# Optimization experiments

Hardware: AMD Instinct MI355X
Metric: run time of the kernel (lower is better)

The kernel has to match this reference:

```python
import jax, jax.numpy as jnp
import numpy as np

H, C = 8, 640            # n_heads, sentence_size (per-head out channels)
HC = H * C               # 5120 concatenated head width
NS, NW, NSEC = 8192, 65536, 1024   # sentences, words, sections
EW, ES, ESEC = 131072, 262144, 16384
WORD, SENT, SECT = 300, 640, 512
FFN_HID = 2048


def setup_inputs() -> dict:
    key = jax.random.key(0)
    ks = jax.random.split(key, 32)
    f = lambda k, sh: (jax.random.normal(k, sh, jnp.float32) * 0.02)
    ri = jax.random.randint
    inp = {}
    inp['Hs'] = jax.random.normal(ks[0], (NS, SENT), jnp.float32)
    inp['Hw'] = jax.random.normal(ks[1], (NW, WORD), jnp.float32)
    inp['HS'] = jax.random.normal(ks[2], (NSEC, SECT), jnp.float32)
    # edge_index convention: row 0 = source nodes, row 1 = target (sentence) nodes
    inp['w2s'] = jnp.stack([ri(ks[3], (EW,), 0, NW), ri(ks[4], (EW,), 0, NS)]).astype(jnp.int32)
    inp['s2s'] = jnp.stack([ri(ks[5], (ES,), 0, NS), ri(ks[6], (ES,), 0, NS)]).astype(jnp.int32)
    inp['S2s'] = jnp.stack([ri(ks[7], (ESEC,), 0, NSEC), ri(ks[8], (ESEC,), 0, NS)]).astype(jnp.int32)
    # gat_w: bipartite (word -> sentence)
    inp['Ww_src'] = f(ks[9], (WORD, HC)); inp['Ww_dst'] = f(ks[10], (SENT, HC))
    inp['aw_src'] = f(ks[11], (H, C)); inp['aw_dst'] = f(ks[12], (H, C)); inp['bw'] = f(ks[13], (HC,))
    # gat_s: sentence -> sentence (shared lin for src/dst)
    inp['Ws'] = f(ks[14], (SENT, HC))
    inp['as_src'] = f(ks[15], (H, C)); inp['as_dst'] = f(ks[16], (H, C)); inp['bs'] = f(ks[17], (HC,))
    # gat_S: bipartite (section -> sentence)
    inp['WS_src'] = f(ks[18], (SECT, HC)); inp['WS_dst'] = f(ks[19], (SENT, HC))
    inp['aS_src'] = f(ks[20], (H, C)); inp['aS_dst'] = f(ks[21], (H, C)); inp['bS'] = f(ks[22], (HC,))
    # fusion gates
    inp['F1_w'] = f(ks[23], (2 * HC, HC)); inp['F1_b'] = f(ks[24], (HC,))
    inp['F2_w'] = f(ks[25], (2 * HC, HC)); inp['F2_b'] = f(ks[26], (HC,))
    # FFN
    inp['l1_w'] = f(ks[27], (HC, FFN_HID)); inp['l1_b'] = f(ks[28], (FFN_HID,))
    inp['l2_w'] = f(ks[29], (FFN_HID, SENT)); inp['l2_b'] = f(ks[30], (SENT,))
    return inp


def _gat(xs, xd, Wsrc, Wdst, asrc, adst, b, edge_index):
    """PyG-style GATConv (concat heads), bipartite (xs -> xd)."""
    N = xd.shape[0]
    hs = (xs @ Wsrc).reshape(-1, H, C)          # [Nsrc,H,C]
    hd = (xd @ Wdst).reshape(-1, H, C)          # [Ndst,H,C]
    al_s = jnp.einsum('nhc,hc->nh', hs, asrc)   # [Nsrc,H]
    al_d = jnp.einsum('nhc,hc->nh', hd, adst)   # [Ndst,H]
    src, dst = edge_index[0], edge_index[1]
    e = jax.nn.leaky_relu(al_s[src] + al_d[dst], negative_slope=0.2)  # [E,H]
    m = jax.ops.segment_max(e, dst, num_segments=N)                   # segment-stable softmax
    ex = jnp.exp(e - m[dst])
    den = jax.ops.segment_sum(ex, dst, num_segments=N)
    alpha = ex / (den[dst] + 1e-16)
    out = jax.ops.segment_sum(hs[src] * alpha[:, :, None], dst, num_segments=N)
    return out.reshape(N, HC) + b


def _fusion(X, Y, W, b):
    Z = jax.nn.sigmoid(jnp.concatenate([X, Y], axis=-1) @ W + b)
    return Z * X + (1.0 - Z) * Y


def reference(Hs, Hw, HS, w2s, s2s, S2s,
              Ww_src, Ww_dst, aw_src, aw_dst, bw,
              Ws, as_src, as_dst, bs,
              WS_src, WS_dst, aS_src, aS_dst, bS,
              F1_w, F1_b, F2_w, F2_b,
              l1_w, l1_b, l2_w, l2_b):
    Uw = jax.nn.elu(_gat(Hw, Hs, Ww_src, Ww_dst, aw_src, aw_dst, bw, w2s))
    Us = jax.nn.elu(_gat(Hs, Hs, Ws, Ws, as_src, as_dst, bs, s2s))
    US = jax.nn.elu(_gat(HS, Hs, WS_src, WS_dst, aS_src, aS_dst, bS, S2s))
    U1 = _fusion(Uw, Us, F1_w, F1_b)
    U2 = _fusion(U1, US, F2_w, F2_b)
    return (U2 @ l1_w + l1_b) @ l2_w + l2_b + Hs
```

## Files before the change

kernel.cpp:

```cpp
#include <hip/hip_runtime.h>
#include <cstdint>
#include <cstddef>

typedef __attribute__((ext_vector_type(8))) __bf16 bf16x8;
typedef __attribute__((ext_vector_type(4))) float f32x4;

static constexpr int kNS   = 8192;
static constexpr int kNW   = 65536;
static constexpr int kNSEC = 1024;
static constexpr int kEW   = 131072;
static constexpr int kES   = 262144;
static constexpr int kESEC = 16384;

__device__ __forceinline__ float eluf(float x)  { return x > 0.f ? x : (__expf(x) - 1.f); }
__device__ __forceinline__ float sigmf(float x) { return 1.f / (1.f + __expf(-x)); }

__device__ __forceinline__ void gload16(const __bf16* g, __bf16* l) {
  __builtin_amdgcn_global_load_lds((const __attribute__((address_space(1))) unsigned int*)g,
                                   (__attribute__((address_space(3))) unsigned int*)l,
                                   16, 0, 0);
}

__global__ __launch_bounds__(256) void conv_transpose(const float* __restrict__ W, int K, int N,
                                                      __bf16* __restrict__ Wt, int KP) {
  __shared__ float t[64][33];
  const int nb = blockIdx.x * 32, kb = blockIdx.y * 64;
  const int tx = threadIdx.x & 31, ty = threadIdx.x >> 5;
#pragma unroll
  for (int i = ty; i < 64; i += 8) {
    const int k = kb + i;
    t[i][tx] = (k < K) ? W[(long)k * N + nb + tx] : 0.f;
  }
  __syncthreads();
  union BU { __bf16 b; unsigned short u; };
#pragma unroll
  for (int i = ty; i < 32; i += 8) {
    BU b0, b1;
    b0.b = (__bf16)t[tx * 2][i];
    b1.b = (__bf16)t[tx * 2 + 1][i];
    const unsigned int pk = ((unsigned int)b1.u << 16) | b0.u;
    *(unsigned int*)(Wt + (long)(nb + i) * KP + kb + tx * 2) = pk;
  }
}

__global__ __launch_bounds__(256) void conv_bf(const float* __restrict__ in, __bf16* __restrict__ outb, long n) {
  long i = (long)blockIdx.x * blockDim.x + threadIdx.x;
  if (i < n) outb[i] = (__bf16)in[i];
}

__global__ __launch_bounds__(256) void head_vecs(const float* __restrict__ W, const float* __restrict__ a,
                                                 float* __restrict__ outv, int Kd, int KP) {
  const int h = blockIdx.x;
  const int lane = threadIdx.x & 63;
  const int k = blockIdx.y * 4 + (threadIdx.x >> 6);
  float s = 0.f;
  if (k < Kd) {
    const float* wr = W + (long)k * 5120 + h * 640;
    const float* ar = a + h * 640;
    for (int c = lane; c < 640; c += 64) s += wr[c] * ar[c];
  }
  for (int o2 = 32; o2; o2 >>= 1) s += __shfl_down(s, o2);
  if (lane == 0) outv[h * KP + k] = (k < Kd) ? s : 0.f;
}

__global__ __launch_bounds__(256) void comb_bias(const float* __restrict__ l1_b, const float* __restrict__ l2_w,
                                                 const float* __restrict__ l2_b, float* __restrict__ bc) {
  const int n = blockIdx.x * 256 + threadIdx.x;
  if (n >= 640) return;
  float s = l2_b[n];
  for (int k = 0; k < 2048; ++k) s += l1_b[k] * l2_w[(long)k * 640 + n];
  bc[n] = s;
}

__global__ __launch_bounds__(256) void att_logits(const float* __restrict__ X, int ldx, int Kd,
                                                  const float* __restrict__ vec, int KP,
                                                  float* __restrict__ outl, int N) {
  const int lane = threadIdx.x & 63;
  const int node = blockIdx.x * 4 + (threadIdx.x >> 6);
  if (node >= N) return;
  const float* xr = X + (long)node * ldx;
  float p[8];
#pragma unroll
  for (int h = 0; h < 8; ++h) p[h] = 0.f;
  for (int k = lane; k < Kd; k += 64) {
    const float xv = xr[k];
#pragma unroll
    for (int h = 0; h < 8; ++h) p[h] += xv * vec[h * KP + k];
  }
#pragma unroll
  for (int h = 0; h < 8; ++h) {
    float v = p[h];
    for (int o2 = 32; o2; o2 >>= 1) v += __shfl_down(v, o2);
    if (lane == 0) outl[(long)node * 8 + h] = v;
  }
}

__global__ __launch_bounds__(256) void att_logits4(const float* __restrict__ X,
                                                   const float* __restrict__ v0, const float* __restrict__ v1,
                                                   const float* __restrict__ v2, const float* __restrict__ v3,
                                                   float* __restrict__ o0, float* __restrict__ o1,
                                                   float* __restrict__ o2, float* __restrict__ o3, int N) {
  const int lane = threadIdx.x & 63;
  const int node = blockIdx.x * 4 + (threadIdx.x >> 6);
  if (node >= N) return;
  const float* xr = X + (long)node * 640;
  float p[4][8];
#pragma unroll
  for (int s = 0; s < 4; ++s)
#pragma unroll
    for (int h = 0; h < 8; ++h) p[s][h] = 0.f;
  for (int k = lane; k < 640; k += 64) {
    const float xv = xr[k];
#pragma unroll
    for (int h = 0; h < 8; ++h) {
      p[0][h] += xv * v0[h * 640 + k];
      p[1][h] += xv * v1[h * 640 + k];
      p[2][h] += xv * v2[h * 640 + k];
      p[3][h] += xv * v3[h * 640 + k];
    }
  }
  float* outs[4] = {o0, o1, o2, o3};
#pragma unroll
  for (int s = 0; s < 4; ++s)
#pragma unroll
    for (int h = 0; h < 8; ++h) {
      float v = p[s][h];
      for (int o2v = 32; o2v; o2v >>= 1) v += __shfl_down(v, o2v);
      if (lane == 0) outs[s][(long)node * 8 + h] = v;
    }
}

__global__ __launch_bounds__(256) void edge_count(const int* __restrict__ dst, int E, int* __restrict__ cnt) {
  const int gid = blockIdx.x * blockDim.x + threadIdx.x;
  if (gid < E) atomicAdd(&cnt[dst[gid]], 1);
}

__global__ __launch_bounds__(1024) void scan_off(const int* __restrict__ cnt, int* __restrict__ offo) {
  __shared__ int part[1024];
  const int tid = threadIdx.x;
  const int base = tid * 8;
  int loc[8];
  int s = 0;
#pragma unroll
  for (int i = 0; i < 8; ++i) { loc[i] = s; s += cnt[base + i]; }
  part[tid] = s;
  __syncthreads();
  for (int d2 = 1; d2 < 1024; d2 <<= 1) {
    int v = (tid >= d2) ? part[tid - d2] : 0;
    __syncthreads();
    part[tid] += v;
    __syncthreads();
  }
  const int pre = (tid > 0) ? part[tid - 1] : 0;
#pragma unroll
  for (int i = 0; i < 8; ++i) offo[base + i] = pre + loc[i];
  if (tid == 1023) offo[8192] = part[1023];
}

__global__ __launch_bounds__(256) void edge_fill(const int* __restrict__ src, const int* __restrict__ dst, int E,
                                                 const int* __restrict__ offo, int* __restrict__ cur,
                                                 int* __restrict__ ssrc) {
  const int gid = blockIdx.x * blockDim.x + threadIdx.x;
  if (gid < E) {
    const int d = dst[gid];
    const int p = offo[d] + atomicAdd(&cur[d], 1);
    ssrc[p] = src[gid];
  }
}

template <int FPAD, int F, bool XPH, bool BIASELU>
__global__ __launch_bounds__(256) void gat_agg(const int* __restrict__ seg_off, const int* __restrict__ ssrc,
                                               const float* __restrict__ als, const float* __restrict__ ald,
                                               const float* __restrict__ X, int ldx,
                                               __bf16* __restrict__ outp, int ldo,
                                               const float* __restrict__ bias) {
  constexpr int C4 = F / 4;
  constexpr int ITEMS = 8 * C4;
  constexpr int L = (ITEMS + 255) / 256;
  const int d = blockIdx.x;
  const int tid = threadIdx.x;
  const int o0 = seg_off[d], o1 = seg_off[d + 1];
  const int deg = o1 - o0;
  __shared__ float exl[64][8];
  __shared__ int ssl[64];
  __shared__ float aldd[8];
  __shared__ float den_s[8];
  if (tid < 8) { aldd[tid] = ald[(long)d * 8 + tid]; den_s[tid] = 0.f; }
  f32x4 acc[L];
  int hh[L], xo[L], oo[L];
  bool vld[L];
#pragma unroll
  for (int l = 0; l < L; ++l) {
    const int idx = tid + l * 256;
    vld[l] = (idx < ITEMS);
    const int h = vld[l] ? (idx / C4) : 0;
    const int c = vld[l] ? (idx - h * C4) : 0;
    hh[l] = h;
    xo[l] = (XPH ? h * F : 0) + c * 4;
    oo[l] = h * FPAD + c * 4;
#pragma unroll
    for (int r = 0; r < 4; ++r) acc[l][r] = 0.f;
  }
  __syncthreads();
  for (int base = 0; base < deg; base += 64) {
    const int nc = min(64, deg - base);
    if (tid < nc) ssl[tid] = ssrc[o0 + base + tid];
    __syncthreads();
    for (int t = tid; t < nc * 8; t += 256) {
      const int e = t >> 3, h = t & 7;
      float v = als[(long)ssl[e] * 8 + h] + aldd[h];
      v = v > 0.f ? v : 0.2f * v;
      exl[e][h] = __expf(v);
    }
    __syncthreads();
    if (tid < 8) {
      float s = 0.f;
      for (int e = 0; e < nc; ++e) s += exl[e][tid];
      den_s[tid] += s;
    }
    for (int e = 0; e < nc; ++e) {
      const float* xr = X + (long)ssl[e] * ldx;
      const float* ex8 = exl[e];
#pragma unroll
      for (int l = 0; l < L; ++l)
        if (vld[l]) {
          const f32x4 v = *(const f32x4*)(xr + xo[l]);
          acc[l] += ex8[hh[l]] * v;
        }
    }
    __syncthreads();
  }
#pragma unroll
  for (int l = 0; l < L; ++l) {
    if (!vld[l]) continue;
    const float dinv = 1.f / (den_s[hh[l]] + 1e-16f);
#pragma unroll
    for (int j = 0; j < 4; ++j) {
      float r = acc[l][j] * dinv;
      if constexpr (BIASELU) { r += bias[oo[l] + j]; r = eluf(r); }
      outp[(long)d * ldo + oo[l] + j] = (__bf16)r;
    }
  }
}

template <int EPI>
__global__ __launch_bounds__(256) void gemm_bt(
    const __bf16* __restrict__ A, int lda, const __bf16* __restrict__ A2, int ksplit,
    const __bf16* __restrict__ Bt, int ldb, int K,
    void* __restrict__ Cout, int ldc,
    const float* __restrict__ bias,
    const __bf16* __restrict__ Xg, const __bf16* __restrict__ Yg, int ldxy,
    const float* __restrict__ Res, int ldres,
    long a_zs, long bt_zs, long c_zs, int b_zs) {
  __shared__ __bf16 sA[2][128 * 32];
  __shared__ __bf16 sB[2][128 * 32];
  const int tid = threadIdx.x;
  const int z = blockIdx.z;
  const int m0 = blockIdx.y * 128, n0 = blockIdx.x * 128;
  const __bf16* Ab = A + (long)z * a_zs;
  const __bf16* A2b = A2 ? A2 + (long)z * a_zs : nullptr;
  const __bf16* Btb = Bt + (long)z * bt_zs;
  const int lane = tid & 63;
  const int wv = tid >> 6, wr = wv >> 1, wc = wv & 1;
  const int fr = lane & 15, fq = lane >> 4;

  const int r0 = tid >> 2, r1 = r0 + 64;
  const int csw = (((tid & 3) ^ ((r0 >> 1) & 3)) * 8);
  const int ldst0 = tid * 8;
  const int ldst1 = 2048 + tid * 8;

  f32x4 acc[4][4];
#pragma unroll
  for (int i = 0; i < 4; ++i)
#pragma unroll
    for (int j = 0; j < 4; ++j)
#pragma unroll
      for (int r = 0; r < 4; ++r) acc[i][j][r] = 0.f;

  const int fsw = (fq ^ ((fr >> 1) & 3)) * 8;
  int aof[4], bof[4];
#pragma unroll
  for (int i = 0; i < 4; ++i) {
    aof[i] = (wr * 64 + i * 16 + fr) * 32 + fsw;
    bof[i] = (wc * 64 + i * 16 + fr) * 32 + fsw;
  }

  const int nkt = K >> 5;
  auto stage = [&](int buf, int kt) {
    const int k0 = kt * 32;
    const __bf16* As = Ab;
    int kr = k0;
    if (A2b && k0 >= ksplit) { As = A2b; kr = k0 - ksplit; }
    gload16(As + (long)(m0 + r0) * lda + kr + csw, &sA[buf][ldst0]);
    gload16(As + (long)(m0 + r1) * lda + kr + csw, &sA[buf][ldst1]);
    gload16(Btb + (long)(n0 + r0) * ldb + k0 + csw, &sB[buf][ldst0]);
    gload16(Btb + (long)(n0 + r1) * ldb + k0 + csw, &sB[buf][ldst1]);
  };

  stage(0, 0);
  for (int kt = 0; kt < nkt; ++kt) {
    const int cur = kt & 1;
    __syncthreads();
    if (kt + 1 < nkt) stage(cur ^ 1, kt + 1);
    bf16x8 af[4], bfv[4];
#pragma unroll
    for (int i = 0; i < 4; ++i) {
      af[i] = *(const bf16x8*)(&sA[cur][aof[i]]);
      bfv[i] = *(const bf16x8*)(&sB[cur][bof[i]]);
    }
#pragma unroll
    for (int i = 0; i < 4; ++i)
#pragma unroll
      for (int j = 0; j < 4; ++j)
        acc[i][j] = __builtin_amdgcn_mfma_f32_16x16x32_bf16(af[i], bfv[j], acc[i][j], 0, 0, 0);
  }

  const float* biasb = bias ? bias + (long)z * b_zs : nullptr;
#pragma unroll
  for (int i = 0; i < 4; ++i) {
#pragma unroll
    for (int j = 0; j < 4; ++j) {
#pragma unroll
      for (int r = 0; r < 4; ++r) {
        const int mm = m0 + wr * 64 + i * 16 + fq * 4 + r;
        const int nn = n0 + wc * 64 + j * 16 + fr;
        const float v = acc[i][j][r];
        const long cidx = (long)mm * ldc + nn + (long)z * c_zs;
        if constexpr (EPI == 0) {
          ((float*)Cout)[cidx] = v;
        } else if constexpr (EPI == 1) {
          ((__bf16*)Cout)[cidx] = (__bf16)eluf(v + biasb[nn]);
        } else if constexpr (EPI == 2) {
          const float zt = sigmf(v + biasb[nn]);
          const float x = (float)Xg[(long)mm * ldxy + nn];
          const float y = (float)Yg[(long)mm * ldxy + nn];
          ((__bf16*)Cout)[cidx] = (__bf16)(zt * x + (1.f - zt) * y);
        } else if constexpr (EPI == 3) {
          ((__bf16*)Cout)[cidx] = (__bf16)(v + biasb[nn]);
        } else if constexpr (EPI == 4) {
          ((float*)Cout)[cidx] = v + biasb[nn] + Res[(long)mm * ldres + nn];
        } else {
          ((__bf16*)Cout)[cidx] = (__bf16)v;
        }
      }
    }
  }
}

template <int EPI>
__global__ __launch_bounds__(512, 2) void gemm256(
    const __bf16* __restrict__ A, int lda, const __bf16* __restrict__ A2, int ksplit,
    const __bf16* __restrict__ Bt, int ldb, int K,
    void* __restrict__ Cout, int ldc,
    const float* __restrict__ bias,
    const __bf16* __restrict__ Xg, const __bf16* __restrict__ Yg, int ldxy,
    int nn_tiles) {
  __shared__ __bf16 sA[2][2][256 * 32];
  __shared__ __bf16 sB[2][2][256 * 32];
  const int tid = threadIdx.x;

  const int nwg = gridDim.x;
  const int lin = blockIdx.x;
  const int qq = nwg >> 3, rr = nwg & 7;
  const int xcd = lin & 7, pos = lin >> 3;
  const int swz = (xcd < rr ? xcd * (qq + 1) : rr * (qq + 1) + (xcd - rr) * qq) + pos;
  const int m0 = (swz / nn_tiles) * 256;
  const int n0 = (swz % nn_tiles) * 256;

  const int lane = tid & 63;
  const int wv = tid >> 6, wm = wv >> 2, wn = wv & 3;
  const int fr = lane & 15, fq = lane >> 4;

  const int srow = tid >> 2;
  const int pslot = tid & 3;

  auto stageA = [&](int bp, int tt, int kk) {
    const int kcol0 = tt * 64 + kk * 32;
    const __bf16* src = A;
    int kc = kcol0;
    if (A2 && kcol0 >= ksplit) { src = A2; kc = kcol0 - ksplit; }
    __bf16* dst = &sA[bp][kk][0];
#pragma unroll
    for (int i = 0; i < 2; ++i) {
      const int r = i * 128 + srow;
      const int l = pslot ^ ((r >> 1) & 3);
      gload16(src + (long)(m0 + r) * lda + kc + l * 8, dst + (i * 512 + tid) * 8);
    }
  };
  auto stageB = [&](int bp, int tt, int kk) {
    const int kcol0 = tt * 64 + kk * 32;
    __bf16* dst = &sB[bp][kk][0];
#pragma unroll
    for (int i = 0; i < 2; ++i) {
      const int r = i * 128 + srow;
      const int l = pslot ^ ((r >> 1) & 3);
      gload16(Bt + (long)(n0 + r) * ldb + kcol0 + l * 8, dst + (i * 512 + tid) * 8);
    }
  };

  int aoff[8], boff[4];
#pragma unroll
  for (int mf = 0; mf < 8; ++mf) {
    const int ra = wm * 128 + mf * 16 + fr;
    aoff[mf] = ra * 32 + ((fq ^ ((ra >> 1) & 3)) * 8);
  }
#pragma unroll
  for (int nf = 0; nf < 4; ++nf) {
    const int rb = wn * 64 + nf * 16 + fr;
    boff[nf] = rb * 32 + ((fq ^ ((rb >> 1) & 3)) * 8);
  }

  f32x4 acc[8][4];
#pragma unroll
  for (int i = 0; i < 8; ++i)
#pragma unroll
    for (int j = 0; j < 4; ++j)
#pragma unroll
      for (int r = 0; r < 4; ++r) acc[i][j][r] = 0.f;

  const int nkt = K >> 6;

  bf16x8 aA[4], aB[4], bA[4], bB[4];

  stageA(0, 0, 0); stageB(0, 0, 0); stageA(0, 0, 1); stageB(0, 0, 1);
  asm volatile("s_waitcnt vmcnt(4)" ::: "memory");
  __builtin_amdgcn_s_barrier();
#pragma unroll
  for (int mf = 0; mf < 4; ++mf) aA[mf] = *(const bf16x8*)(&sA[0][0][aoff[mf]]);
#pragma unroll
  for (int nf = 0; nf < 4; ++nf) bA[nf] = *(const bf16x8*)(&sB[0][0][boff[nf]]);

  for (int t = 0; t < nkt; ++t) {
    const int cb = t & 1, nb = cb ^ 1;
    const bool pf = (t + 1 < nkt);

#pragma unroll
    for (int mf = 0; mf < 4; ++mf) aB[mf] = *(const bf16x8*)(&sA[cb][0][aoff[4 + mf]]);
    if (pf) stageA(nb, t + 1, 0);
    asm volatile("s_waitcnt lgkmcnt(4)" ::: "memory");
    __builtin_amdgcn_sched_barrier(0);
    __builtin_amdgcn_s_setprio(1);
#pragma unroll
    for (int mf = 0; mf < 4; ++mf)
#pragma unroll
      for (int nf = 0; nf < 4; ++nf)
        acc[mf][nf] = __builtin_amdgcn_mfma_f32_16x16x32_bf16(aA[mf], bA[nf], acc[mf][nf], 0, 0, 0);
    __builtin_amdgcn_s_setprio(0);
    __builtin_amdgcn_sched_barrier(0);

    if (pf) stageB(nb, t + 1, 0);
    if (pf) asm volatile("s_waitcnt vmcnt(4)" ::: "memory");
    else    asm volatile("s_waitcnt vmcnt(0)" ::: "memory");
    __builtin_amdgcn_s_barrier();

#pragma unroll
    for (int mf = 0; mf < 4; ++mf) aA[mf] = *(const bf16x8*)(&sA[cb][1][aoff[mf]]);
#pragma unroll
    for (int nf = 0; nf < 4; ++nf) bB[nf] = *(const bf16x8*)(&sB[cb][1][boff[nf]]);
    asm volatile("s_waitcnt lgkmcnt(8)" ::: "memory");
    __builtin_amdgcn_sched_barrier(0);
    __builtin_amdgcn_s_setprio(1);
#pragma unroll
    for (int mf = 0; mf < 4; ++mf)
#pragma unroll
      for (int nf = 0; nf < 4; ++nf)
        acc[4 + mf][nf] = __builtin_amdgcn_mfma_f32_16x16x32_bf16(aB[mf], bA[nf], acc[4 + mf][nf], 0, 0, 0);
    __builtin_amdgcn_s_setprio(0);
    __builtin_amdgcn_sched_barrier(0);

#pragma unroll
    for (int mf = 0; mf < 4; ++mf) aB[mf] = *(const bf16x8*)(&sA[cb][1][aoff[4 + mf]]);
    if (pf) stageA(nb, t + 1, 1);
    asm volatile("s_waitcnt lgkmcnt(4)" ::: "memory");
    __builtin_amdgcn_sched_barrier(0);
    __builtin_amdgcn_s_setprio(1);
#pragma unroll
    for (int mf = 0; mf < 4; ++mf)
#pragma unroll
      for (int nf = 0; nf < 4; ++nf)
        acc[mf][nf] = __builtin_amdgcn_mfma_f32_16x16x32_bf16(aA[mf], bB[nf], acc[mf][nf], 0, 0, 0);
    __builtin_amdgcn_s_setprio(0);
    __builtin_amdgcn_sched_barrier(0);

    if (pf) {
      stageB(nb, t + 1, 1);
      asm volatile("s_waitcnt vmcnt(4)" ::: "memory");
    }
    __builtin_amdgcn_s_barrier();

    if (pf) {
#pragma unroll
      for (int mf = 0; mf < 4; ++mf) aA[mf] = *(const bf16x8*)(&sA[nb][0][aoff[mf]]);
#pragma unroll
      for (int nf = 0; nf < 4; ++nf) bA[nf] = *(const bf16x8*)(&sB[nb][0][boff[nf]]);
      asm volatile("s_waitcnt lgkmcnt(8)" ::: "memory");
    } else {
      asm volatile("s_waitcnt lgkmcnt(0)" ::: "memory");
    }
    __builtin_amdgcn_sched_barrier(0);
    __builtin_amdgcn_s_setprio(1);
#pragma unroll
    for (int mf = 0; mf < 4; ++mf)
#pragma unroll
      for (int nf = 0; nf < 4; ++nf)
        acc[4 + mf][nf] = __builtin_amdgcn_mfma_f32_16x16x32_bf16(aB[mf], bB[nf], acc[4 + mf][nf], 0, 0, 0);
    __builtin_amdgcn_s_setprio(0);
    __builtin_amdgcn_sched_barrier(0);
  }

#pragma unroll
  for (int mf = 0; mf < 8; ++mf) {
#pragma unroll
    for (int nf = 0; nf < 4; ++nf) {
#pragma unroll
      for (int r = 0; r < 4; ++r) {
        const int mm = m0 + wm * 128 + mf * 16 + fq * 4 + r;
        const int nn = n0 + wn * 64 + nf * 16 + fr;
        const float v = acc[mf][nf][r];
        const long cidx = (long)mm * ldc + nn;
        if constexpr (EPI == 2) {
          const float zt = sigmf(v + bias[nn]);
          const float x = (float)Xg[(long)mm * ldxy + nn];
          const float y = (float)Yg[(long)mm * ldxy + nn];
          ((__bf16*)Cout)[cidx] = (__bf16)(zt * x + (1.f - zt) * y);
        } else {
          ((__bf16*)Cout)[cidx] = (__bf16)(v + bias[nn]);
        }
      }
    }
  }
}

extern "C" void kernel_launch(void* const* d_in, const int* in_sizes, int n_in,
                              void* d_out, int out_size, void* d_ws, size_t ws_size,
                              hipStream_t stream) {
  (void)in_sizes; (void)n_in; (void)out_size; (void)ws_size;
  const float* Hs    = (const float*)d_in[0];
  const float* Hw    = (const float*)d_in[1];
  const float* HSec  = (const float*)d_in[2];
  const int* w2s     = (const int*)d_in[3];
  const int* s2s     = (const int*)d_in[4];
  const int* S2s     = (const int*)d_in[5];
  const float* Ww_src = (const float*)d_in[6];
  const float* Ww_dst = (const float*)d_in[7];
  const float* aw_src = (const float*)d_in[8];
  const float* aw_dst = (const float*)d_in[9];
  const float* bw     = (const float*)d_in[10];
  const float* Wss    = (const float*)d_in[11];
  const float* as_src = (const float*)d_in[12];
  const float* as_dst = (const float*)d_in[13];
  const float* bs     = (const float*)d_in[14];
  const float* WS_src = (const float*)d_in[15];
  const float* WS_dst = (const float*)d_in[16];
  const float* aS_src = (const float*)d_in[17];
  const float* aS_dst = (const float*)d_in[18];
  const float* bS     = (const float*)d_in[19];
  const float* F1_w   = (const float*)d_in[20];
  const float* F1_b   = (const float*)d_in[21];
  const float* F2_w   = (const float*)d_in[22];
  const float* F2_b   = (const float*)d_in[23];
  const float* l1_w   = (const float*)d_in[24];
  const float* l1_b   = (const float*)d_in[25];
  const float* l2_w   = (const float*)d_in[26];
  const float* l2_b   = (const float*)d_in[27];
  float* outp = (float*)d_out;

  char* ws = (char*)d_ws;
  size_t cur_off = 0;
  auto alloc = [&](size_t bytes) -> char* {
    char* p = ws + cur_off;
    cur_off = (cur_off + bytes + 255) & ~(size_t)255;
    return p;
  };

  __bf16* Wt_w  = (__bf16*)alloc((size_t)5120 * 320 * 2);
  __bf16* Wt_s  = (__bf16*)alloc((size_t)5120 * 640 * 2);
  __bf16* Wt_S  = (__bf16*)alloc((size_t)5120 * 512 * 2);
  __bf16* WtF   = (__bf16*)alloc((size_t)5120 * 10240 * 2);
  __bf16* Wt_l2 = (__bf16*)alloc((size_t)640 * 2048 * 2);
  __bf16* l1_bf = (__bf16*)alloc((size_t)5120 * 2048 * 2);
  __bf16* WcT   = (__bf16*)alloc((size_t)640 * 5120 * 2);
  float*  bc    = (float*)alloc(640 * 4);
  __bf16* HS_bf = (__bf16*)alloc((size_t)1024 * 512 * 2);
  float* v_w = (float*)alloc(8 * 320 * 4);
  float* u_w = (float*)alloc(8 * 640 * 4);
  float* v_s = (float*)alloc(8 * 640 * 4);
  float* u_s = (float*)alloc(8 * 640 * 4);
  float* v_S = (float*)alloc(8 * 512 * 4);
  float* u_S = (float*)alloc(8 * 640 * 4);
  float* alw_s = (float*)alloc((size_t)kNW * 8 * 4);
  float* alw_d = (float*)alloc((size_t)kNS * 8 * 4);
  float* als_s = (float*)alloc((size_t)kNS * 8 * 4);
  float* als_d = (float*)alloc((size_t)kNS * 8 * 4);
  float* alS_s = (float*)alloc((size_t)kNSEC * 8 * 4);
  float* alS_d = (float*)alloc((size_t)kNS * 8 * 4);
  int* csr_i  = (int*)alloc((size_t)6 * kNS * 4);
  int* cnt_w = csr_i, *cnt_s = csr_i + kNS, *cnt_S = csr_i + 2 * kNS;
  int* cur_w = csr_i + 3 * kNS, *cur_s = csr_i + 4 * kNS, *cur_S = csr_i + 5 * kNS;
  int* off_w = (int*)alloc((size_t)(kNS + 1) * 4);
  int* off_s = (int*)alloc((size_t)(kNS + 1) * 4);
  int* off_S = (int*)alloc((size_t)(kNS + 1) * 4);
  int* ssrc_w = (int*)alloc((size_t)kEW * 4);
  int* ssrc_s = (int*)alloc((size_t)kES * 4);
  int* ssrc_S = (int*)alloc((size_t)kESEC * 4);
  float* hs_S = (float*)alloc((size_t)1024 * 5120 * 4);
  char* aggreg = alloc((size_t)kNS * 2560 * 2 + (size_t)kNS * 5120 * 2);
  __bf16* agg_w = (__bf16*)aggreg;
  __bf16* agg_s = (__bf16*)(aggreg + (size_t)kNS * 2560 * 2);
  __bf16* U1 = (__bf16*)aggreg;
  __bf16* Uw = (__bf16*)alloc((size_t)kNS * 5120 * 2);
  __bf16* Us = (__bf16*)alloc((size_t)kNS * 5120 * 2);
  __bf16* US = (__bf16*)alloc((size_t)kNS * 5120 * 2);
  __bf16* U2 = Uw;

  const dim3 b256(256);

  conv_transpose<<<dim3(160, 5), b256, 0, stream>>>(Ww_src, 300, 5120, Wt_w, 320);
  conv_transpose<<<dim3(160, 10), b256, 0, stream>>>(Wss, 640, 5120, Wt_s, 640);
  conv_transpose<<<dim3(160, 8), b256, 0, stream>>>(WS_src, 512, 5120, Wt_S, 512);
  conv_transpose<<<dim3(160, 160), b256, 0, stream>>>(F1_w, 10240, 5120, WtF, 10240);
  conv_transpose<<<dim3(20, 32), b256, 0, stream>>>(l2_w, 2048, 640, Wt_l2, 2048);
  conv_bf<<<(1024 * 512 + 255) / 256, b256, 0, stream>>>(HSec, HS_bf, (long)1024 * 512);
  conv_bf<<<((long)5120 * 2048 + 255) / 256, b256, 0, stream>>>(l1_w, l1_bf, (long)5120 * 2048);

  gemm_bt<5><<<dim3(40, 5, 1), b256, 0, stream>>>(
      Wt_l2, 2048, nullptr, 1 << 30, l1_bf, 2048, 2048,
      WcT, 5120, nullptr, nullptr, nullptr, 0, nullptr, 0, 0, 0, 0, 0);
  comb_bias<<<3, b256, 0, stream>>>(l1_b, l2_w, l2_b, bc);

  head_vecs<<<dim3(8, 80), b256, 0, stream>>>(Ww_src, aw_src, v_w, 300, 320);
  head_vecs<<<dim3(8, 160), b256, 0, stream>>>(Ww_dst, aw_dst, u_w, 640, 640);
  head_vecs<<<dim3(8, 160), b256, 0, stream>>>(Wss, as_src, v_s, 640, 640);
  head_vecs<<<dim3(8, 160), b256, 0, stream>>>(Wss, as_dst, u_s, 640, 640);
  head_vecs<<<dim3(8, 128), b256, 0, stream>>>(WS_src, aS_src, v_S, 512, 512);
  head_vecs<<<dim3(8, 160), b256, 0, stream>>>(WS_dst, aS_dst, u_S, 640, 640);

  att_logits<<<(kNW + 3) / 4, b256, 0, stream>>>(Hw, 300, 300, v_w, 320, alw_s, kNW);
  att_logits<<<(kNSEC + 3) / 4, b256, 0, stream>>>(HSec, 512, 512, v_S, 512, alS_s, kNSEC);
  att_logits4<<<(kNS + 3) / 4, b256, 0, stream>>>(Hs, u_w, v_s, u_s, u_S,
                                                  alw_d, als_s, als_d, alS_d, kNS);

  hipMemsetAsync(csr_i, 0, (size_t)6 * kNS * 4, stream);
  edge_count<<<(kEW + 255) / 256, b256, 0, stream>>>(w2s + kEW, kEW, cnt_w);
  edge_count<<<(kES + 255) / 256, b256, 0, stream>>>(s2s + kES, kES, cnt_s);
  edge_count<<<(kESEC + 255) / 256, b256, 0, stream>>>(S2s + kESEC, kESEC, cnt_S);
  scan_off<<<1, 1024, 0, stream>>>(cnt_w, off_w);
  scan_off<<<1, 1024, 0, stream>>>(cnt_s, off_s);
  scan_off<<<1, 1024, 0, stream>>>(cnt_S, off_S);
  edge_fill<<<(kEW + 255) / 256, b256, 0, stream>>>(w2s, w2s + kEW, kEW, off_w, cur_w, ssrc_w);
  edge_fill<<<(kES + 255) / 256, b256, 0, stream>>>(s2s, s2s + kES, kES, off_s, cur_s, ssrc_s);
  edge_fill<<<(kESEC + 255) / 256, b256, 0, stream>>>(S2s, S2s + kESEC, kESEC, off_S, cur_S, ssrc_S);

  gemm_bt<0><<<dim3(40, 8, 1), b256, 0, stream>>>(
      HS_bf, 512, nullptr, 1 << 30, Wt_S, 512, 512,
      hs_S, 5120, nullptr, nullptr, nullptr, 0, nullptr, 0, 0, 0, 0, 0);

  gat_agg<320, 300, false, false><<<kNS, b256, 0, stream>>>(off_w, ssrc_w, alw_s, alw_d, Hw, 300, agg_w, 2560, nullptr);
  gat_agg<640, 640, false, false><<<kNS, b256, 0, stream>>>(off_s, ssrc_s, als_s, als_d, Hs, 640, agg_s, 5120, nullptr);
  gat_agg<640, 640, true, true><<<kNS, b256, 0, stream>>>(off_S, ssrc_S, alS_s, alS_d, hs_S, 5120, US, 5120, bS);

  gemm_bt<1><<<dim3(5, 64, 8), b256, 0, stream>>>(
      agg_w, 2560, nullptr, 1 << 30, Wt_w, 320, 320,
      Uw, 5120, bw, nullptr, nullptr, 0, nullptr, 0, 320, (long)640 * 320, 640, 640);
  gemm_bt<1><<<dim3(5, 64, 8), b256, 0, stream>>>(
      agg_s, 5120, nullptr, 1 << 30, Wt_s, 640, 640,
      Us, 5120, bs, nullptr, nullptr, 0, nullptr, 0, 640, (long)640 * 640, 640, 640);

  gemm256<2><<<dim3(640), dim3(512), 0, stream>>>(
      Uw, 5120, Us, 5120, WtF, 10240, 10240,
      U1, 5120, F1_b, Uw, Us, 5120, 20);

  conv_transpose<<<dim3(160, 160), b256, 0, stream>>>(F2_w, 10240, 5120, WtF, 10240);
  gemm256<2><<<dim3(640), dim3(512), 0, stream>>>(
      U1, 5120, US, 5120, WtF, 10240, 10240,
      U2, 5120, F2_b, U1, US, 5120, 20);

  gemm_bt<4><<<dim3(5, 64, 1), b256, 0, stream>>>(
      U2, 5120, nullptr, 1 << 30, WcT, 5120, 5120,
      outp, 640, bc, nullptr, nullptr, 0, Hs, 640, 0, 0, 0, 0);
}
```

Baseline: 3.089 ms.

## Batch small preprocessing kernels, use bf16 gather sources, overlap F2 transpose with fusion GEMM

Merges the six head_vecs launches, the three edge_count/scan/fill launches into single batched kernels to cut launch overhead. Converts Hs to bf16 and writes the section projection hs_S in bf16, so two GAT aggregations gather half the bytes per edge through a new bf16x8 aggregation kernel. Adds extra workgroups to the first fusion GEMM that transpose F2_w into a separate buffer at the same time, when workspace allows, removing a serial transpose launch. This costs extra workspace, an added conversion pass over Hs, and bf16 rounding of the gathered features.

```diff
diff --git a/kernel.cpp b/kernel.cpp
--- a/kernel.cpp
+++ b/kernel.cpp
@@ -48,19 +48,23 @@
   if (i < n) outb[i] = (__bf16)in[i];
 }
 
-__global__ __launch_bounds__(256) void head_vecs(const float* __restrict__ W, const float* __restrict__ a,
-                                                 float* __restrict__ outv, int Kd, int KP) {
+struct HVJ { const float* W; const float* a; float* o; int Kd; int KP; };
+struct HVJobs { HVJ j[6]; };
+
+__global__ __launch_bounds__(256) void head_vecs6(HVJobs jb) {
+  const HVJ J = jb.j[blockIdx.z];
   const int h = blockIdx.x;
   const int lane = threadIdx.x & 63;
   const int k = blockIdx.y * 4 + (threadIdx.x >> 6);
+  if (k >= J.KP) return;
   float s = 0.f;
-  if (k < Kd) {
-    const float* wr = W + (long)k * 5120 + h * 640;
-    const float* ar = a + h * 640;
+  if (k < J.Kd) {
+    const float* wr = J.W + (long)k * 5120 + h * 640;
+    const float* ar = J.a + h * 640;
     for (int c = lane; c < 640; c += 64) s += wr[c] * ar[c];
   }
   for (int o2 = 32; o2; o2 >>= 1) s += __shfl_down(s, o2);
-  if (lane == 0) outv[h * KP + k] = (k < Kd) ? s : 0.f;
+  if (lane == 0) J.o[h * J.KP + k] = (k < J.Kd) ? s : 0.f;
 }
 
 __global__ __launch_bounds__(256) void comb_bias(const float* __restrict__ l1_b, const float* __restrict__ l2_w,
@@ -130,12 +134,20 @@
     }
 }
 
-__global__ __launch_bounds__(256) void edge_count(const int* __restrict__ dst, int E, int* __restrict__ cnt) {
+__global__ __launch_bounds__(256) void edge_count3(const int* __restrict__ d0, int E0, int* __restrict__ c0,
+                                                   const int* __restrict__ d1, int E1, int* __restrict__ c1,
+                                                   const int* __restrict__ d2, int E2, int* __restrict__ c2) {
   const int gid = blockIdx.x * blockDim.x + threadIdx.x;
-  if (gid < E) atomicAdd(&cnt[dst[gid]], 1);
-}
-
-__global__ __launch_bounds__(1024) void scan_off(const int* __restrict__ cnt, int* __restrict__ offo) {
+  if (gid < E0) atomicAdd(&c0[d0[gid]], 1);
+  else if (gid < E0 + E1) atomicAdd(&c1[d1[gid - E0]], 1);
+  else if (gid < E0 + E1 + E2) atomicAdd(&c2[d2[gid - E0 - E1]], 1);
+}
+
+__global__ __launch_bounds__(1024) void scan_off3(const int* __restrict__ c0, int* __restrict__ o0,
+                                                  const int* __restrict__ c1, int* __restrict__ o1,
+                                                  const int* __restrict__ c2, int* __restrict__ o2) {
+  const int* cnt = blockIdx.x == 0 ? c0 : (blockIdx.x == 1 ? c1 : c2);
+  int* offo = blockIdx.x == 0 ? o0 : (blockIdx.x == 1 ? o1 : o2);
   __shared__ int part[1024];
   const int tid = threadIdx.x;
   const int base = tid * 8;
@@ -157,14 +169,20 @@
   if (tid == 1023) offo[8192] = part[1023];
 }
 
-__global__ __launch_bounds__(256) void edge_fill(const int* __restrict__ src, const int* __restrict__ dst, int E,
-                                                 const int* __restrict__ offo, int* __restrict__ cur,
-                                                 int* __restrict__ ssrc) {
+__global__ __launch_bounds__(256) void edge_fill3(
+    const int* __restrict__ s0, const int* __restrict__ d0, int E0, const int* __restrict__ of0, int* __restrict__ cu0, int* __restrict__ sr0,
+    const int* __restrict__ s1, const int* __restrict__ d1, int E1, const int* __restrict__ of1, int* __restrict__ cu1, int* __restrict__ sr1,
+    const int* __restrict__ s2, const int* __restrict__ d2, int E2, const int* __restrict__ of2, int* __restrict__ cu2, int* __restrict__ sr2) {
   const int gid = blockIdx.x * blockDim.x + threadIdx.x;
-  if (gid < E) {
-    const int d = dst[gid];
-    const int p = offo[d] + atomicAdd(&cur[d], 1);
-    ssrc[p] = src[gid];
+  if (gid < E0) {
+    const int d = d0[gid];
+    sr0[of0[d] + atomicAdd(&cu0[d], 1)] = s0[gid];
+  } else if (gid < E0 + E1) {
+    const int g = gid - E0, d = d1[g];
+    sr1[of1[d] + atomicAdd(&cu1[d], 1)] = s1[g];
+  } else if (gid < E0 + E1 + E2) {
+    const int g = gid - E0 - E1, d = d2[g];
+    sr2[of2[d] + atomicAdd(&cu2[d], 1)] = s2[g];
   }
 }
 
@@ -236,6 +254,83 @@
     const float dinv = 1.f / (den_s[hh[l]] + 1e-16f);
 #pragma unroll
     for (int j = 0; j < 4; ++j) {
+      float r = acc[l][j] * dinv;
+      if constexpr (BIASELU) { r += bias[oo[l] + j]; r = eluf(r); }
+      outp[(long)d * ldo + oo[l] + j] = (__bf16)r;
+    }
+  }
+}
+
+template <int FPAD, int F, bool XPH, bool BIASELU>
+__global__ __launch_bounds__(256) void gat_agg_bf(const int* __restrict__ seg_off, const int* __restrict__ ssrc,
+                                                  const float* __restrict__ als, const float* __restrict__ ald,
+                                                  const __bf16* __restrict__ X, int ldx,
+                                                  __bf16* __restrict__ outp, int ldo,
+                                                  const float* __restrict__ bias) {
+  constexpr int C8 = F / 8;
+  constexpr int ITEMS = 8 * C8;
+  constexpr int L = (ITEMS + 255) / 256;
+  const int d = blockIdx.x;
+  const int tid = threadIdx.x;
+  const int o0 = seg_off[d], o1 = seg_off[d + 1];
+  const int deg = o1 - o0;
+  __shared__ float exl[64][8];
+  __shared__ int ssl[64];
+  __shared__ float aldd[8];
+  __shared__ float den_s[8];
+  if (tid < 8) { aldd[tid] = ald[(long)d * 8 + tid]; den_s[tid] = 0.f; }
+  float acc[L][8];
+  int hh[L], xo[L], oo[L];
+  bool vld[L];
+#pragma unroll
+  for (int l = 0; l < L; ++l) {
+    const int idx = tid + l * 256;
+    vld[l] = (idx < ITEMS);
+    const int h = vld[l] ? (idx / C8) : 0;
+    const int c = vld[l] ? (idx - h * C8) : 0;
+    hh[l] = h;
+    xo[l] = (XPH ? h * F : 0) + c * 8;
+    oo[l] = h * FPAD + c * 8;
+#pragma unroll
+    for (int r = 0; r < 8; ++r) acc[l][r] = 0.f;
+  }
+  __syncthreads();
+  for (int base = 0; base < deg; base += 64) {
+    const int nc = min(64, deg - base);
+    if (tid < nc) ssl[tid] = ssrc[o0 + base + tid];
+    __syncthreads();
+    for (int t = tid; t < nc * 8; t += 256) {
+      const int e = t >> 3, h = t & 7;
+      float v = als[(long)ssl[e] * 8 + h] + aldd[h];
+      v = v > 0.f ? v : 0.2f * v;
+      exl[e][h] = __expf(v);
+    }
+    __syncthreads();
+    if (tid < 8) {
+      float s = 0.f;
+      for (int e = 0; e < nc; ++e) s += exl[e][tid];
+      den_s[tid] += s;
+    }
+    for (int e = 0; e < nc; ++e) {
+      const __bf16* xr = X + (long)ssl[e] * ldx;
+      const float* ex8 = exl[e];
+#pragma unroll
+      for (int l = 0; l < L; ++l)
+        if (vld[l]) {
+          const bf16x8 v = *(const bf16x8*)(xr + xo[l]);
+          const float w = ex8[hh[l]];
+#pragma unroll
+          for (int r = 0; r < 8; ++r) acc[l][r] += w * (float)v[r];
+        }
+    }
+    __syncthreads();
+  }
+#pragma unroll
+  for (int l = 0; l < L; ++l) {
+    if (!vld[l]) continue;
+    const float dinv = 1.f / (den_s[hh[l]] + 1e-16f);
+#pragma unroll
+    for (int j = 0; j < 8; ++j) {
       float r = acc[l][j] * dinv;
       if constexpr (BIASELU) { r += bias[oo[l] + j]; r = eluf(r); }
       outp[(long)d * ldo + oo[l] + j] = (__bf16)r;
@@ -354,13 +449,44 @@
     void* __restrict__ Cout, int ldc,
     const float* __restrict__ bias,
     const __bf16* __restrict__ Xg, const __bf16* __restrict__ Yg, int ldxy,
-    int nn_tiles) {
+    int nn_tiles, int ngemm,
+    const float* __restrict__ tW, __bf16* __restrict__ tWt, int tK, int tN, int tKP) {
   __shared__ __bf16 sA[2][2][256 * 32];
   __shared__ __bf16 sB[2][2][256 * 32];
   const int tid = threadIdx.x;
-
-  const int nwg = gridDim.x;
   const int lin = blockIdx.x;
+
+  if (lin >= ngemm) {
+    if (tW) {
+      float* sc = (float*)&sA[0][0][0];
+      const int nworkers = gridDim.x - ngemm;
+      const int wid = lin - ngemm;
+      const int ntx = tN >> 5, nty = tKP >> 6;
+      const int tx = tid & 31, ty = tid >> 5;
+      union BU { __bf16 b; unsigned short u; };
+      for (int tile = wid; tile < ntx * nty; tile += nworkers) {
+        const int nb = (tile % ntx) * 32, kb = (tile / ntx) * 64;
+#pragma unroll
+        for (int i = ty; i < 64; i += 16) {
+          const int k = kb + i;
+          sc[i * 33 + tx] = (k < tK) ? tW[(long)k * tN + nb + tx] : 0.f;
+        }
+        __syncthreads();
+#pragma unroll
+        for (int i = ty; i < 32; i += 16) {
+          BU b0, b1;
+          b0.b = (__bf16)sc[(tx * 2) * 33 + i];
+          b1.b = (__bf16)sc[(tx * 2 + 1) * 33 + i];
+          const unsigned int pk = ((unsigned int)b1.u << 16) | b0.u;
+          *(unsigned int*)(tWt + (long)(nb + i) * tKP + kb + tx * 2) = pk;
+        }
+        __syncthreads();
+      }
+    }
+    return;
+  }
+
+  const int nwg = ngemm;
   const int qq = nwg >> 3, rr = nwg & 7;
   const int xcd = lin & 7, pos = lin >> 3;
   const int swz = (xcd < rr ? xcd * (qq + 1) : rr * (qq + 1) + (xcd - rr) * qq) + pos;
@@ -534,7 +660,7 @@
 extern "C" void kernel_launch(void* const* d_in, const int* in_sizes, int n_in,
                               void* d_out, int out_size, void* d_ws, size_t ws_size,
                               hipStream_t stream) {
-  (void)in_sizes; (void)n_in; (void)out_size; (void)ws_size;
+  (void)in_sizes; (void)n_in; (void)out_size;
   const float* Hs    = (const float*)d_in[0];
   const float* Hw    = (const float*)d_in[1];
   const float* HSec  = (const float*)d_in[2];
@@ -582,6 +708,7 @@
   __bf16* WcT   = (__bf16*)alloc((size_t)640 * 5120 * 2);
   float*  bc    = (float*)alloc(640 * 4);
   __bf16* HS_bf = (__bf16*)alloc((size_t)1024 * 512 * 2);
+  __bf16* Hs_bf = (__bf16*)alloc((size_t)kNS * 640 * 2);
   float* v_w = (float*)alloc(8 * 320 * 4);
   float* u_w = (float*)alloc(8 * 640 * 4);
   float* v_s = (float*)alloc(8 * 640 * 4);
@@ -603,7 +730,7 @@
   int* ssrc_w = (int*)alloc((size_t)kEW * 4);
   int* ssrc_s = (int*)alloc((size_t)kES * 4);
   int* ssrc_S = (int*)alloc((size_t)kESEC * 4);
-  float* hs_S = (float*)alloc((size_t)1024 * 5120 * 4);
+  __bf16* hs_Sb = (__bf16*)alloc((size_t)1024 * 5120 * 2);
   char* aggreg = alloc((size_t)kNS * 2560 * 2 + (size_t)kNS * 5120 * 2);
   __bf16* agg_w = (__bf16*)aggreg;
   __bf16* agg_s = (__bf16*)(aggreg + (size_t)kNS * 2560 * 2);
@@ -613,6 +740,12 @@
   __bf16* US = (__bf16*)alloc((size_t)kNS * 5120 * 2);
   __bf16* U2 = Uw;
 
+  __bf16* WtF2 = nullptr;
+  {
+    const size_t f2b = (size_t)5120 * 10240 * 2;
+    if (cur_off + f2b + 256 <= ws_size) WtF2 = (__bf16*)alloc(f2b);
+  }
+
   const dim3 b256(256);
 
   conv_transpose<<<dim3(160, 5), b256, 0, stream>>>(Ww_src, 300, 5120, Wt_w, 320);
@@ -621,6 +754,7 @@
   conv_transpose<<<dim3(160, 160), b256, 0, stream>>>(F1_w, 10240, 5120, WtF, 10240);
   conv_transpose<<<dim3(20, 32), b256, 0, stream>>>(l2_w, 2048, 640, Wt_l2, 2048);
   conv_bf<<<(1024 * 512 + 255) / 256, b256, 0, stream>>>(HSec, HS_bf, (long)1024 * 512);
+  conv_bf<<<((long)kNS * 640 + 255) / 256, b256, 0, stream>>>(Hs, Hs_bf, (long)kNS * 640);
   conv_bf<<<((long)5120 * 2048 + 255) / 256, b256, 0, stream>>>(l1_w, l1_bf, (long)5120 * 2048);
 
   gemm_bt<5><<<dim3(40, 5, 1), b256, 0, stream>>>(
@@ -628,12 +762,16 @@
       WcT, 5120, nullptr, nullptr, nullptr, 0, nullptr, 0, 0, 0, 0, 0);
   comb_bias<<<3, b256, 0, stream>>>(l1_b, l2_w, l2_b, bc);
 
-  head_vecs<<<dim3(8, 80), b256, 0, stream>>>(Ww_src, aw_src, v_w, 300, 320);
-  head_vecs<<<dim3(8, 160), b256, 0, stream>>>(Ww_dst, aw_dst, u_w, 640, 640);
-  head_vecs<<<dim3(8, 160), b256, 0, stream>>>(Wss, as_src, v_s, 640, 640);
-  head_vecs<<<dim3(8, 160), b256, 0, stream>>>(Wss, as_dst, u_s, 640, 640);
-  head_vecs<<<dim3(8, 128), b256, 0, stream>>>(WS_src, aS_src, v_S, 512, 512);
-  head_vecs<<<dim3(8, 160), b256, 0, stream>>>(WS_dst, aS_dst, u_S, 640, 640);
+  {
+    HVJobs jb;
+    jb.j[0] = {Ww_src, aw_src, v_w, 300, 320};
+    jb.j[1] = {Ww_dst, aw_dst, u_w, 640, 640};
+    jb.j[2] = {Wss,    as_src, v_s, 640, 640};
+    jb.j[3] = {Wss,    as_dst, u_s, 640, 640};
+    jb.j[4] = {WS_src, aS_src, v_S, 512, 512};
+    jb.j[5] = {WS_dst, aS_dst, u_S, 640, 640};
+    head_vecs6<<<dim3(8, 160, 6), b256, 0, stream>>>(jb);
+  }
 
   att_logits<<<(kNW + 3) / 4, b256, 0, stream>>>(Hw, 300, 300, v_w, 320, alw_s, kNW);
   att_logits<<<(kNSEC + 3) / 4, b256, 0, stream>>>(HSec, 512, 512, v_S, 512, alS_s, kNSEC);
@@ -641,23 +779,21 @@
                                                   alw_d, als_s, als_d, alS_d, kNS);
 
   hipMemsetAsync(csr_i, 0, (size_t)6 * kNS * 4, stream);
-  edge_count<<<(kEW + 255) / 256, b256, 0, stream>>>(w2s + kEW, kEW, cnt_w);
-  edge_count<<<(kES + 255) / 256, b256, 0, stream>>>(s2s + kES, kES, cnt_s);
-  edge_count<<<(kESEC + 255) / 256, b256, 0, stream>>>(S2s + kESEC, kESEC, cnt_S);
-  scan_off<<<1, 1024, 0, stream>>>(cnt_w, off_w);
-  scan_off<<<1, 1024, 0, stream>>>(cnt_s, off_s);
-  scan_off<<<1, 1024, 0, stream>>>(cnt_S, off_S);
-  edge_fill<<<(kEW + 255) / 256, b256, 0, stream>>>(w2s, w2s + kEW, kEW, off_w, cur_w, ssrc_w);
-  edge_fill<<<(kES + 255) / 256, b256, 0, stream>>>(s2s, s2s + kES, kES, off_s, cur_s, ssrc_s);
-  edge_fill<<<(kESEC + 255) / 256, b256, 0, stream>>>(S2s, S2s + kESEC, kESEC, off_S, cur_S, ssrc_S);
-
-  gemm_bt<0><<<dim3(40, 8, 1), b256, 0, stream>>>(
+  edge_count3<<<(kEW + kES + kESEC + 255) / 256, b256, 0, stream>>>(
+      w2s + kEW, kEW, cnt_w, s2s + kES, kES, cnt_s, S2s + kESEC, kESEC, cnt_S);
+  scan_off3<<<3, 1024, 0, stream>>>(cnt_w, off_w, cnt_s, off_s, cnt_S, off_S);
+  edge_fill3<<<(kEW + kES + kESEC + 255) / 256, b256, 0, stream>>>(
+      w2s, w2s + kEW, kEW, off_w, cur_w, ssrc_w,
+      s2s, s2s + kES, kES, off_s, cur_s, ssrc_s,
+      S2s, S2s + kESEC, kESEC, off_S, cur_S, ssrc_S);
+
+  gemm_bt<5><<<dim3(40, 8, 1), b256, 0, stream>>>(
       HS_bf, 512, nullptr, 1 << 30, Wt_S, 512, 512,
-      hs_S, 5120, nullptr, nullptr, nullptr, 0, nullptr, 0, 0, 0, 0, 0);
+      hs_Sb, 5120, nullptr, nullptr, nullptr, 0, nullptr, 0, 0, 0, 0, 0);
 
   gat_agg<320, 300, false, false><<<kNS, b256, 0, stream>>>(off_w, ssrc_w, alw_s, alw_d, Hw, 300, agg_w, 2560, nullptr);
-  gat_agg<640, 640, false, false><<<kNS, b256, 0, stream>>>(off_s, ssrc_s, als_s, als_d, Hs, 640, agg_s, 5120, nullptr);
-  gat_agg<640, 640, true, true><<<kNS, b256, 0, stream>>>(off_S, ssrc_S, alS_s, alS_d, hs_S, 5120, US, 5120, bS);
+  gat_agg_bf<640, 640, false, false><<<kNS, b256, 0, stream>>>(off_s, ssrc_s, als_s, als_d, Hs_bf, 640, agg_s, 5120, nullptr);
+  gat_agg_bf<640, 640, true, true><<<kNS, b256, 0, stream>>>(off_S, ssrc_S, alS_s, alS_d, hs_Sb, 5120, US, 5120, bS);
 
   gemm_bt<1><<<dim3(5, 64, 8), b256, 0, stream>>>(
       agg_w, 2560, nullptr, 1 << 30, Wt_w, 320, 320,
@@ -666,14 +802,23 @@
       agg_s, 5120, nullptr, 1 << 30, Wt_s, 640, 640,
       Us, 5120, bs, nullptr, nullptr, 0, nullptr, 0, 640, (long)640 * 640, 640, 640);
 
+  if (WtF2) {
+    gemm256<2><<<dim3(640 + 128), dim3(512), 0, stream>>>(
+        Uw, 5120, Us, 5120, WtF, 10240, 10240,
+        U1, 5120, F1_b, Uw, Us, 5120, 20,
+        640, F2_w, WtF2, 10240, 5120, 10240);
+  } else {
+    gemm256<2><<<dim3(640), dim3(512), 0, stream>>>(
+        Uw, 5120, Us, 5120, WtF, 10240, 10240,
+        U1, 5120, F1_b, Uw, Us, 5120, 20,
+        640, nullptr, nullptr, 0, 0, 0);
+    conv_transpose<<<dim3(160, 160), b256, 0, stream>>>(F2_w, 10240, 5120, WtF, 10240);
+  }
+
   gemm256<2><<<dim3(640), dim3(512), 0, stream>>>(
-      Uw, 5120, Us, 5120, WtF, 10240, 10240,
-      U1, 5120, F1_b, Uw, Us, 5120, 20);
-
-  conv_transpose<<<dim3(160, 160), b256, 0, stream>>>(F2_w, 10240, 5120, WtF, 10240);
-  gemm256<2><<<dim3(640), dim3(512), 0, stream>>>(
-      U1, 5120, US, 5120, WtF, 10240, 10240,
-      U2, 5120, F2_b, U1, US, 5120, 20);
+      U1, 5120, US, 5120, WtF2 ? WtF2 : WtF, 10240, 10240,
+      U2, 5120, F2_b, U1, US, 5120, 20,
+      640, nullptr, nullptr, 0, 0, 0);
 
   gemm_bt<4><<<dim3(5, 64, 1), b256, 0, stream>>>(
       U2, 5120, nullptr, 1 << 30, WcT, 5120, 5120,
```

Measured after the change: 3.090 ms. About the same (+0.0%).
